# Kernel tuning notes

Hardware: AMD Instinct MI355X
Metric: run time of the kernel (lower is better)

## Reference

```python
import jax, jax.numpy as jnp
import numpy as np

D_MODEL = 2048
NUM_HEADS = 16
HEAD_DIM = D_MODEL // NUM_HEADS


def setup_inputs() -> dict:
    key = jax.random.key(0)
    ks = jax.random.split(key, 11)
    B, S = 2, 2048
    s = 1.0 / np.sqrt(D_MODEL)
    return {
        "query": jax.random.normal(ks[0], (B, S, D_MODEL), jnp.float32),
        "key_in": jax.random.normal(ks[1], (B, S, D_MODEL), jnp.float32),
        "value": jax.random.normal(ks[2], (B, S, D_MODEL), jnp.float32),
        "Wq": jax.random.normal(ks[3], (D_MODEL, D_MODEL), jnp.float32) * s,
        "bq": jnp.zeros((D_MODEL,), jnp.float32),
        "Wk": jax.random.normal(ks[4], (D_MODEL, D_MODEL), jnp.float32) * s,
        "bk": jnp.zeros((D_MODEL,), jnp.float32),
        "Wv": jax.random.normal(ks[5], (D_MODEL, D_MODEL), jnp.float32) * s,
        "bv": jnp.zeros((D_MODEL,), jnp.float32),
        "Wo": jax.random.normal(ks[6], (D_MODEL, D_MODEL), jnp.float32) * s,
        "bo": jnp.zeros((D_MODEL,), jnp.float32),
    }


def reference(query, key_in, value, Wq, bq, Wk, bk, Wv, bv, Wo, bo):
    B, S, _ = query.shape
    # projections (torch Linear: x @ W.T + b)
    q = query @ Wq.T + bq
    k = key_in @ Wk.T + bk
    v = value @ Wv.T + bv
    # [B, H, S, Dh]
    q = q.reshape(B, S, NUM_HEADS, HEAD_DIM).transpose(0, 2, 1, 3)
    k = k.reshape(B, -1, NUM_HEADS, HEAD_DIM).transpose(0, 2, 1, 3)
    v = v.reshape(B, -1, NUM_HEADS, HEAD_DIM).transpose(0, 2, 1, 3)
    scores = jnp.einsum("bhqd,bhkd->bhqk", q, k) / np.sqrt(HEAD_DIM).astype(np.float32)
    attn = jax.nn.softmax(scores, axis=-1)
    out = jnp.einsum("bhqk,bhkd->bhqd", attn, v)
    out = out.transpose(0, 2, 1, 3).reshape(B, S, D_MODEL)
    return out @ Wo.T + bo
```

## Files before the change

### kernel.cpp

```cpp
#include <hip/hip_runtime.h>
#include <hip/hip_bf16.h>
#include <stdint.h>

typedef __hip_bfloat16 bf16;
typedef __attribute__((ext_vector_type(8))) short bf16x8;
typedef __attribute__((ext_vector_type(4))) float f32x4;
typedef __attribute__((ext_vector_type(4))) short s16x4;

constexpr int D_MODEL   = 2048;
constexpr int NUM_HEADS = 16;
constexpr int HEAD_DIM  = 128;
constexpr int BATCH     = 2;
constexpr int SEQ       = 2048;

__device__ __forceinline__ void gload_lds16(const bf16* g, bf16* l) {
    __builtin_amdgcn_global_load_lds(
        (const __attribute__((address_space(1))) void*)g,
        (__attribute__((address_space(3))) void*)l, 16, 0, 0);
}

struct CvtArgs { const float* src[7]; bf16* dst[7]; int n8[7]; };

__global__ __launch_bounds__(256)
void cvt_multi(CvtArgs a)
{
    const int t = blockIdx.y;
    const float* __restrict__ s = a.src[t];
    bf16* __restrict__ d = a.dst[t];
    const int n8 = a.n8[t];
    for (int i = blockIdx.x * 256 + threadIdx.x; i < n8; i += gridDim.x * 256) {
        f32x4 x = *(const f32x4*)(s + (size_t)i * 8);
        f32x4 y = *(const f32x4*)(s + (size_t)i * 8 + 4);
        bf16 t8[8] = { __float2bfloat16(x[0]), __float2bfloat16(x[1]),
                       __float2bfloat16(x[2]), __float2bfloat16(x[3]),
                       __float2bfloat16(y[0]), __float2bfloat16(y[1]),
                       __float2bfloat16(y[2]), __float2bfloat16(y[3]) };
        *(bf16x8*)(d + (size_t)i * 8) = *(const bf16x8*)t8;
    }
}

template <typename TC, bool TRANS_PERM>
__device__ __forceinline__
void gemm_body(const bf16* __restrict__ A, const bf16* __restrict__ W,
               const float* __restrict__ bias, TC* __restrict__ C,
               int M, int N, int K)
{
    constexpr int BM = 128, BN = 128, BK = 32;
    __shared__ bf16 sA[BM][BK];
    __shared__ bf16 sB[BN][BK];

    const int tid  = threadIdx.x;
    const int wave = tid >> 6, lane = tid & 63;
    const int quad = lane >> 4, l16 = lane & 15;
    const int wr = wave >> 1, wc = wave & 1;
    const int m0 = blockIdx.y * BM, n0 = blockIdx.x * BN;
    bf16* sAf = &sA[0][0];
    bf16* sBf = &sB[0][0];

    f32x4 acc[4][4];
#pragma unroll
    for (int i = 0; i < 4; i++)
#pragma unroll
        for (int j = 0; j < 4; j++) acc[i][j] = (f32x4){0.f, 0.f, 0.f, 0.f};

    for (int k0 = 0; k0 < K; k0 += BK) {
        __syncthreads();
#pragma unroll
        for (int s = 0; s < 2; s++) {
            int c = s * 256 + wave * 64 + lane;
            int row = c >> 2, col = (c & 3) * 8;
            gload_lds16(&A[(size_t)(m0 + row) * K + k0 + col], sAf + (size_t)c * 8);
            gload_lds16(&W[(size_t)(n0 + row) * K + k0 + col], sBf + (size_t)c * 8);
        }
        __syncthreads();

        bf16x8 af[4], bfr[4];
#pragma unroll
        for (int i = 0; i < 4; i++) af[i]  = *(const bf16x8*)&sA[wr * 64 + i * 16 + l16][quad * 8];
#pragma unroll
        for (int j = 0; j < 4; j++) bfr[j] = *(const bf16x8*)&sB[wc * 64 + j * 16 + l16][quad * 8];
#pragma unroll
        for (int i = 0; i < 4; i++)
#pragma unroll
            for (int j = 0; j < 4; j++)
                acc[i][j] = __builtin_amdgcn_mfma_f32_16x16x32_bf16(af[i], bfr[j], acc[i][j], 0, 0, 0);
    }

#pragma unroll
    for (int j = 0; j < 4; j++) {
        int col = n0 + wc * 64 + j * 16 + l16;
        float bv = bias[col];
#pragma unroll
        for (int i = 0; i < 4; i++) {
            if constexpr (TRANS_PERM) {
                int row0 = m0 + wr * 64 + i * 16 + quad * 4;
                int g    = row0 & 63;
                int tau  = g >> 4, qh = (g >> 2) & 3;
                int pp   = (tau >> 1) * 32 + qh * 8 + (tau & 1) * 4;
                int sp   = ((row0 & 2047) & ~63) | pp;
                size_t idx = (size_t)(row0 >> 11) * ((size_t)D_MODEL * SEQ)
                           + (size_t)col * SEQ + sp;
                bf16 t4[4];
#pragma unroll
                for (int r = 0; r < 4; r++) t4[r] = __float2bfloat16(acc[i][j][r] + bv);
                *(s16x4*)&C[idx] = *(const s16x4*)t4;
            } else {
#pragma unroll
                for (int r = 0; r < 4; r++) {
                    int row = m0 + wr * 64 + i * 16 + quad * 4 + r;
                    if constexpr (sizeof(TC) == 2)
                        C[(size_t)row * N + col] = (TC)__float2bfloat16(acc[i][j][r] + bv);
                    else
                        C[(size_t)row * N + col] = (TC)(acc[i][j][r] + bv);
                }
            }
        }
    }
}

template <typename TC, bool TRANS_PERM>
__global__ __launch_bounds__(256, 2)
void gemm_bf16(const bf16* __restrict__ A, const bf16* __restrict__ W,
               const float* __restrict__ bias, TC* __restrict__ C,
               int M, int N, int K)
{
    gemm_body<TC, TRANS_PERM>(A, W, bias, C, M, N, K);
}

struct QkvArgs { const bf16* A[3]; const bf16* W[3]; const float* bias[3]; bf16* C[3]; };

__global__ __launch_bounds__(256, 2)
void gemm_qkv(QkvArgs ga, int M, int N, int K)
{
    const int z = blockIdx.z;
    if (z == 2) gemm_body<bf16, true >(ga.A[2], ga.W[2], ga.bias[2], ga.C[2], M, N, K);
    else        gemm_body<bf16, false>(ga.A[z], ga.W[z], ga.bias[z], ga.C[z], M, N, K);
}

struct QkArgs { const bf16* A[2]; const bf16* W[2]; const float* bias[2]; bf16* C[2]; };

__global__ __launch_bounds__(256, 2)
void gemm_qk(QkArgs ga, int M, int N, int K)
{
    const int z = blockIdx.z;
    gemm_body<bf16, false>(ga.A[z], ga.W[z], ga.bias[z], ga.C[z], M, N, K);
}

__global__ __launch_bounds__(256)
void flash_attn_kernel(const bf16* __restrict__ Qp, const bf16* __restrict__ Kp,
                       const bf16* __restrict__ Vt, bf16* __restrict__ Op)
{
    constexpr int BQ = 128, BKV = 64, DH = 128;
    __shared__ bf16 sK[2][BKV * DH];
    __shared__ bf16 sV[2][DH * BKV];

    const int tid  = threadIdx.x;
    const int wave = tid >> 6, lane = tid & 63;
    const int quad = lane >> 4, l16 = lane & 15;
    const int q0 = blockIdx.x * BQ;
    const int h  = blockIdx.y;
    const int b  = blockIdx.z;

    const size_t base  = (size_t)b * SEQ * D_MODEL + (size_t)h * HEAD_DIM;
    const size_t basev = ((size_t)b * NUM_HEADS + h) * (size_t)HEAD_DIM * SEQ;
    const bf16* Kb = Kp + base;
    const bf16* Vb = Vt + basev;

    auto stage = [&](int t, int bi) {
        const bf16* Kt = Kb + (size_t)t * BKV * D_MODEL;
        const bf16* Vtile = Vb + (size_t)t * BKV;
        bf16* sKb = sK[bi];
        bf16* sVb = sV[bi];
#pragma unroll
        for (int s = 0; s < 4; s++) {
            int c = s * 256 + wave * 64 + lane;
            int row = c >> 4, gs = c & 15;
            int g = gs ^ (row & 15);
            gload_lds16(Kt + (size_t)row * D_MODEL + g * 8, sKb + (size_t)c * 8);
        }
#pragma unroll
        for (int s = 0; s < 4; s++) {
            int c = s * 256 + wave * 64 + lane;
            int dh = c >> 3, gs = c & 7;
            int g = gs ^ (dh & 7);
            gload_lds16(Vtile + (size_t)dh * SEQ + g * 8, sVb + (size_t)c * 8);
        }
    };

    bf16x8 bq[2][4];
#pragma unroll
    for (int nt = 0; nt < 2; nt++)
#pragma unroll
        for (int kk = 0; kk < 4; kk++)
            bq[nt][kk] = *(const bf16x8*)&Qp[base +
                (size_t)(q0 + wave * 32 + nt * 16 + l16) * D_MODEL + kk * 32 + quad * 8];

    f32x4 oacc[2][8];
#pragma unroll
    for (int nt = 0; nt < 2; nt++)
#pragma unroll
        for (int mt = 0; mt < 8; mt++) oacc[nt][mt] = (f32x4){0.f, 0.f, 0.f, 0.f};

    float lsum[2] = {0.f, 0.f};

    const float SCL2E = 0.08838834764831845f * 1.4426950408889634f;
    constexpr int NT = SEQ / BKV;

    stage(0, 0);

    for (int t = 0; t < NT; ++t) {
        __syncthreads();
        if (t + 1 < NT) stage(t + 1, (t + 1) & 1);

        const bf16* sKc = sK[t & 1];
        const bf16* sVc = sV[t & 1];

        f32x4 sacc[2][4];
#pragma unroll
        for (int nt = 0; nt < 2; nt++)
#pragma unroll
            for (int kt = 0; kt < 4; kt++) sacc[nt][kt] = (f32x4){0.f, 0.f, 0.f, 0.f};
#pragma unroll
        for (int kk = 0; kk < 4; kk++) {
            bf16x8 ak[4];
#pragma unroll
            for (int kt = 0; kt < 4; kt++) {
                int row = kt * 16 + l16;
                int g   = (kk * 4 + quad) ^ l16;
                ak[kt] = *(const bf16x8*)&sKc[(size_t)row * DH + g * 8];
            }
#pragma unroll
            for (int nt = 0; nt < 2; nt++)
#pragma unroll
                for (int kt = 0; kt < 4; kt++)
                    sacc[nt][kt] = __builtin_amdgcn_mfma_f32_16x16x32_bf16(ak[kt], bq[nt][kk], sacc[nt][kt], 0, 0, 0);
        }

        bf16x8 pb[2][2];
#pragma unroll
        for (int nt = 0; nt < 2; nt++) {
            bf16 tmp[16];
#pragma unroll
            for (int kt = 0; kt < 4; kt++) {
#pragma unroll
                for (int r = 0; r < 4; r++) {
                    float p = exp2f(fminf(sacc[nt][kt][r] * SCL2E, 60.f));
                    lsum[nt] += p;
                    tmp[(kt >> 1) * 8 + (kt & 1) * 4 + r] = __float2bfloat16(p);
                }
            }
            pb[nt][0] = *(const bf16x8*)&tmp[0];
            pb[nt][1] = *(const bf16x8*)&tmp[8];
        }

#pragma unroll
        for (int c = 0; c < 2; c++) {
#pragma unroll
            for (int mt = 0; mt < 8; mt++) {
                int row = mt * 16 + l16;
                int g   = (c * 4 + quad) ^ (l16 & 7);
                bf16x8 av = *(const bf16x8*)&sVc[(size_t)row * BKV + g * 8];
#pragma unroll
                for (int nt = 0; nt < 2; nt++)
                    oacc[nt][mt] = __builtin_amdgcn_mfma_f32_16x16x32_bf16(av, pb[nt][c], oacc[nt][mt], 0, 0, 0);
            }
        }
    }

#pragma unroll
    for (int nt = 0; nt < 2; nt++) {
        float v = lsum[nt];
        v += __shfl_xor(v, 16);
        v += __shfl_xor(v, 32);
        lsum[nt] = v;
    }

#pragma unroll
    for (int nt = 0; nt < 2; nt++) {
        float inv = 1.f / lsum[nt];
        int row = q0 + wave * 32 + nt * 16 + l16;
#pragma unroll
        for (int mt = 0; mt < 8; mt++) {
            bf16 t4[4];
#pragma unroll
            for (int r = 0; r < 4; r++) t4[r] = __float2bfloat16(oacc[nt][mt][r] * inv);
            *(s16x4*)&Op[base + (size_t)row * D_MODEL + mt * 16 + quad * 4] = *(const s16x4*)t4;
        }
    }
}

extern "C" void kernel_launch(void* const* d_in, const int* in_sizes, int n_in,
                              void* d_out, int out_size, void* d_ws, size_t ws_size,
                              hipStream_t stream)
{
    const float* query  = (const float*)d_in[0];
    const float* key_in = (const float*)d_in[1];
    const float* value  = (const float*)d_in[2];
    const float* Wq = (const float*)d_in[3];
    const float* bq = (const float*)d_in[4];
    const float* Wk = (const float*)d_in[5];
    const float* bk = (const float*)d_in[6];
    const float* Wv = (const float*)d_in[7];
    const float* bv = (const float*)d_in[8];
    const float* Wo = (const float*)d_in[9];
    const float* bo = (const float*)d_in[10];
    float* out = (float*)d_out;

    const int tokens = BATCH * SEQ;
    const size_t nAct = (size_t)tokens * D_MODEL;
    const size_t nW   = (size_t)D_MODEL * D_MODEL;

    const bool fused_qkv = ws_size >= (6 * nAct + 4 * nW) * sizeof(bf16);

    bf16* p = (bf16*)d_ws;
    bf16* qb  = p; p += nAct;
    bf16* kb  = p; p += nAct;
    bf16* vb  = p; p += nAct;
    bf16* wqb = p; p += nW;
    bf16* wkb = p; p += nW;
    bf16* wvb = p; p += nW;
    bf16* wob = p; p += nW;
    bf16* qp  = p; p += nAct;
    bf16* kp  = p; p += nAct;
    bf16* vpT;
    if (fused_qkv) { vpT = p; p += nAct; }
    else           { vpT = qb; }
    bf16* ap = fused_qkv ? qb : kb;

    CvtArgs ca;
    ca.src[0] = query;  ca.dst[0] = qb;  ca.n8[0] = (int)(nAct / 8);
    ca.src[1] = key_in; ca.dst[1] = kb;  ca.n8[1] = (int)(nAct / 8);
    ca.src[2] = value;  ca.dst[2] = vb;  ca.n8[2] = (int)(nAct / 8);
    ca.src[3] = Wq;     ca.dst[3] = wqb; ca.n8[3] = (int)(nW / 8);
    ca.src[4] = Wk;     ca.dst[4] = wkb; ca.n8[4] = (int)(nW / 8);
    ca.src[5] = Wv;     ca.dst[5] = wvb; ca.n8[5] = (int)(nW / 8);
    ca.src[6] = Wo;     ca.dst[6] = wob; ca.n8[6] = (int)(nW / 8);
    cvt_multi<<<dim3(512, 7), 256, 0, stream>>>(ca);

    if (fused_qkv) {
        QkvArgs qa;
        qa.A[0] = qb; qa.W[0] = wqb; qa.bias[0] = bq; qa.C[0] = qp;
        qa.A[1] = kb; qa.W[1] = wkb; qa.bias[1] = bk; qa.C[1] = kp;
        qa.A[2] = vb; qa.W[2] = wvb; qa.bias[2] = bv; qa.C[2] = vpT;
        dim3 g3(D_MODEL / 128, tokens / 128, 3);
        gemm_qkv<<<g3, 256, 0, stream>>>(qa, tokens, D_MODEL, D_MODEL);
    } else {
        QkArgs qa;
        qa.A[0] = qb; qa.W[0] = wqb; qa.bias[0] = bq; qa.C[0] = qp;
        qa.A[1] = kb; qa.W[1] = wkb; qa.bias[1] = bk; qa.C[1] = kp;
        dim3 g2(D_MODEL / 128, tokens / 128, 2);
        gemm_qk<<<g2, 256, 0, stream>>>(qa, tokens, D_MODEL, D_MODEL);
        dim3 gg(D_MODEL / 128, tokens / 128);
        gemm_bf16<bf16, true><<<gg, 256, 0, stream>>>(vb, wvb, bv, vpT, tokens, D_MODEL, D_MODEL);
    }

    dim3 ga(SEQ / 128, NUM_HEADS, BATCH);
    flash_attn_kernel<<<ga, 256, 0, stream>>>(qp, kp, vpT, ap);

    dim3 gg(D_MODEL / 128, tokens / 128);
    gemm_bf16<float, false><<<gg, 256, 0, stream>>>(ap, wob, bo, out, tokens, D_MODEL, D_MODEL);
}
```

Before: 481.1 us.

## Rewrite projection GEMMs with 256x128 tiles, triple-buffered LDS and swizzled loads

Replaces the single-buffered 128x128x32 GEMM with a 512-thread 256x128x64 tile that triple-buffers A and B in LDS via direct global-to-LDS loads. Data for step t+2 is prefetched while four interleaved MFMA phases run, with XOR-swizzled LDS addressing to avoid bank conflicts and s_setprio around the MFMA bursts. The goal is to hide global load latency and cut the per-k-step barrier stalls of the old loop. In exchange each block uses much more LDS (about 144 KB) and registers, leaving one block per CU, and the grid has half as many blocks. Correctness rests on hand-placed vmcnt waits and barriers.

```diff
diff --git a/kernel.cpp b/kernel.cpp
--- a/kernel.cpp
+++ b/kernel.cpp
@@ -12,6 +12,12 @@
 constexpr int HEAD_DIM  = 128;
 constexpr int BATCH     = 2;
 constexpr int SEQ       = 2048;
+
+constexpr int GBM = 256, GBN = 128, GBK = 64;
+constexpr int G_ABUF = GBM * GBK;
+constexpr int G_BBUF = GBN * GBK;
+constexpr int G_BUF  = G_ABUF + G_BBUF;
+constexpr int G_LDS  = 3 * G_BUF;
 
 __device__ __forceinline__ void gload_lds16(const bf16* g, bf16* l) {
     __builtin_amdgcn_global_load_lds(
@@ -39,23 +45,52 @@
     }
 }
 
+template <int P>
+__device__ __forceinline__
+void phase_mfma(f32x4 (&acc)[4][4], bf16x8 (&a)[4][2], bf16x8 (&b)[4][2])
+{
+#pragma unroll
+    for (int kk = 0; kk < 2; kk++) {
+#pragma unroll
+        for (int j = 0; j <= P; j++)
+            acc[P][j] = __builtin_amdgcn_mfma_f32_16x16x32_bf16(a[P][kk], b[j][kk], acc[P][j], 0, 0, 0);
+#pragma unroll
+        for (int i = 0; i < P; i++)
+            acc[i][P] = __builtin_amdgcn_mfma_f32_16x16x32_bf16(a[i][kk], b[P][kk], acc[i][P], 0, 0, 0);
+    }
+}
+
 template <typename TC, bool TRANS_PERM>
 __device__ __forceinline__
 void gemm_body(const bf16* __restrict__ A, const bf16* __restrict__ W,
                const float* __restrict__ bias, TC* __restrict__ C,
-               int M, int N, int K)
-{
-    constexpr int BM = 128, BN = 128, BK = 32;
-    __shared__ bf16 sA[BM][BK];
-    __shared__ bf16 sB[BN][BK];
-
+               int M, int N, int K, bf16* smem)
+{
     const int tid  = threadIdx.x;
-    const int wave = tid >> 6, lane = tid & 63;
+    const int lane = tid & 63;
+    const int wave = tid >> 6;
     const int quad = lane >> 4, l16 = lane & 15;
-    const int wr = wave >> 1, wc = wave & 1;
-    const int m0 = blockIdx.y * BM, n0 = blockIdx.x * BN;
-    bf16* sAf = &sA[0][0];
-    bf16* sBf = &sB[0][0];
+    const int sw   = l16 & 7;
+    const int wr   = wave >> 1;
+    const int wc   = wave & 1;
+    const int m0   = blockIdx.y * GBM, n0 = blockIdx.x * GBN;
+
+    const int rloc = tid >> 3;
+    const int gsw  = (tid & 7) ^ (rloc & 7);
+    const int NT   = K / GBK;
+
+    const bf16* Abase = A + (size_t)(m0 + rloc) * K + gsw * 8;
+    const bf16* Bbase = W + (size_t)(n0 + rloc) * K + gsw * 8;
+    const size_t rstep = (size_t)64 * K;
+
+    auto stageA = [&](int t, int bi, int u) {
+        gload_lds16(Abase + u * rstep + (size_t)t * GBK,
+                    smem + bi * G_BUF + (u * 512 + tid) * 8);
+    };
+    auto stageB = [&](int t, int bi, int u) {
+        gload_lds16(Bbase + u * rstep + (size_t)t * GBK,
+                    smem + bi * G_BUF + G_ABUF + (u * 512 + tid) * 8);
+    };
 
     f32x4 acc[4][4];
 #pragma unroll
@@ -63,41 +98,71 @@
 #pragma unroll
         for (int j = 0; j < 4; j++) acc[i][j] = (f32x4){0.f, 0.f, 0.f, 0.f};
 
-    for (int k0 = 0; k0 < K; k0 += BK) {
-        __syncthreads();
-#pragma unroll
-        for (int s = 0; s < 2; s++) {
-            int c = s * 256 + wave * 64 + lane;
-            int row = c >> 2, col = (c & 3) * 8;
-            gload_lds16(&A[(size_t)(m0 + row) * K + k0 + col], sAf + (size_t)c * 8);
-            gload_lds16(&W[(size_t)(n0 + row) * K + k0 + col], sBf + (size_t)c * 8);
-        }
-        __syncthreads();
-
-        bf16x8 af[4], bfr[4];
-#pragma unroll
-        for (int i = 0; i < 4; i++) af[i]  = *(const bf16x8*)&sA[wr * 64 + i * 16 + l16][quad * 8];
-#pragma unroll
-        for (int j = 0; j < 4; j++) bfr[j] = *(const bf16x8*)&sB[wc * 64 + j * 16 + l16][quad * 8];
-#pragma unroll
-        for (int i = 0; i < 4; i++)
-#pragma unroll
-            for (int j = 0; j < 4; j++)
-                acc[i][j] = __builtin_amdgcn_mfma_f32_16x16x32_bf16(af[i], bfr[j], acc[i][j], 0, 0, 0);
-    }
+    bf16x8 a[4][2], b[4][2];
+
+#pragma unroll
+    for (int u = 0; u < 4; u++) stageA(0, 0, u);
+#pragma unroll
+    for (int u = 0; u < 2; u++) stageB(0, 0, u);
+    if (NT > 1) {
+#pragma unroll
+        for (int u = 0; u < 4; u++) stageA(1, 1, u);
+#pragma unroll
+        for (int u = 0; u < 2; u++) stageB(1, 1, u);
+        asm volatile("s_waitcnt vmcnt(6)" ::: "memory");
+    } else {
+        asm volatile("s_waitcnt vmcnt(0)" ::: "memory");
+    }
+    asm volatile("s_barrier" ::: "memory");
+
+#define GEMM_PHASE(p, STAGE_STMT)                                              \
+    {                                                                          \
+        STAGE_STMT;                                                            \
+        const int rA = wr * 64 + (p) * 16 + l16;                               \
+        const int rB = wc * 64 + (p) * 16 + l16;                               \
+        a[p][0] = *(const bf16x8*)&sAc[rA * 64 + (quad ^ sw) * 8];             \
+        a[p][1] = *(const bf16x8*)&sAc[rA * 64 + (((4 + quad) ^ sw)) * 8];     \
+        b[p][0] = *(const bf16x8*)&sBc[rB * 64 + (quad ^ sw) * 8];             \
+        b[p][1] = *(const bf16x8*)&sBc[rB * 64 + (((4 + quad) ^ sw)) * 8];     \
+        __builtin_amdgcn_s_barrier();                                          \
+        __builtin_amdgcn_s_setprio(1);                                         \
+        phase_mfma<p>(acc, a, b);                                              \
+        __builtin_amdgcn_s_setprio(0);                                         \
+    }
+
+    int bc = 0;
+    for (int t = 0; t < NT; ++t) {
+        const bf16* sAc = smem + bc * G_BUF;
+        const bf16* sBc = sAc + G_ABUF;
+        const int bs = (bc + 2 >= 3) ? bc - 1 : bc + 2;
+        const bool pf = (t + 2 < NT);
+
+        GEMM_PHASE(0, if (pf) { stageA(t + 2, bs, 0); stageA(t + 2, bs, 1); })
+        __builtin_amdgcn_s_barrier();
+        GEMM_PHASE(1, if (pf) { stageA(t + 2, bs, 2); stageA(t + 2, bs, 3); })
+        __builtin_amdgcn_s_barrier();
+        GEMM_PHASE(2, if (pf) { stageB(t + 2, bs, 0); })
+        __builtin_amdgcn_s_barrier();
+        GEMM_PHASE(3, if (pf) { stageB(t + 2, bs, 1); })
+        if (pf)                asm volatile("s_waitcnt vmcnt(6)" ::: "memory");
+        else if (t + 1 < NT)   asm volatile("s_waitcnt vmcnt(0)" ::: "memory");
+        asm volatile("s_barrier" ::: "memory");
+        bc = (bc + 1 == 3) ? 0 : bc + 1;
+    }
+#undef GEMM_PHASE
 
 #pragma unroll
     for (int j = 0; j < 4; j++) {
-        int col = n0 + wc * 64 + j * 16 + l16;
-        float bv = bias[col];
+        const int col = n0 + wc * 64 + j * 16 + l16;
+        const float bv = bias[col];
 #pragma unroll
         for (int i = 0; i < 4; i++) {
+            const int row0 = m0 + wr * 64 + i * 16 + quad * 4;
             if constexpr (TRANS_PERM) {
-                int row0 = m0 + wr * 64 + i * 16 + quad * 4;
-                int g    = row0 & 63;
-                int tau  = g >> 4, qh = (g >> 2) & 3;
-                int pp   = (tau >> 1) * 32 + qh * 8 + (tau & 1) * 4;
-                int sp   = ((row0 & 2047) & ~63) | pp;
+                int g   = row0 & 63;
+                int tau = g >> 4, qh = (g >> 2) & 3;
+                int pp  = (tau >> 1) * 32 + qh * 8 + (tau & 1) * 4;
+                int sp  = ((row0 & 2047) & ~63) | pp;
                 size_t idx = (size_t)(row0 >> 11) * ((size_t)D_MODEL * SEQ)
                            + (size_t)col * SEQ + sp;
                 bf16 t4[4];
@@ -107,7 +172,7 @@
             } else {
 #pragma unroll
                 for (int r = 0; r < 4; r++) {
-                    int row = m0 + wr * 64 + i * 16 + quad * 4 + r;
+                    int row = row0 + r;
                     if constexpr (sizeof(TC) == 2)
                         C[(size_t)row * N + col] = (TC)__float2bfloat16(acc[i][j][r] + bv);
                     else
@@ -119,31 +184,34 @@
 }
 
 template <typename TC, bool TRANS_PERM>
-__global__ __launch_bounds__(256, 2)
+__global__ __launch_bounds__(512, 1)
 void gemm_bf16(const bf16* __restrict__ A, const bf16* __restrict__ W,
                const float* __restrict__ bias, TC* __restrict__ C,
                int M, int N, int K)
 {
-    gemm_body<TC, TRANS_PERM>(A, W, bias, C, M, N, K);
+    __shared__ bf16 smem[G_LDS];
+    gemm_body<TC, TRANS_PERM>(A, W, bias, C, M, N, K, smem);
 }
 
 struct QkvArgs { const bf16* A[3]; const bf16* W[3]; const float* bias[3]; bf16* C[3]; };
 
-__global__ __launch_bounds__(256, 2)
+__global__ __launch_bounds__(512, 1)
 void gemm_qkv(QkvArgs ga, int M, int N, int K)
 {
+    __shared__ bf16 smem[G_LDS];
     const int z = blockIdx.z;
-    if (z == 2) gemm_body<bf16, true >(ga.A[2], ga.W[2], ga.bias[2], ga.C[2], M, N, K);
-    else        gemm_body<bf16, false>(ga.A[z], ga.W[z], ga.bias[z], ga.C[z], M, N, K);
+    if (z == 2) gemm_body<bf16, true >(ga.A[2], ga.W[2], ga.bias[2], ga.C[2], M, N, K, smem);
+    else        gemm_body<bf16, false>(ga.A[z], ga.W[z], ga.bias[z], ga.C[z], M, N, K, smem);
 }
 
 struct QkArgs { const bf16* A[2]; const bf16* W[2]; const float* bias[2]; bf16* C[2]; };
 
-__global__ __launch_bounds__(256, 2)
+__global__ __launch_bounds__(512, 1)
 void gemm_qk(QkArgs ga, int M, int N, int K)
 {
+    __shared__ bf16 smem[G_LDS];
     const int z = blockIdx.z;
-    gemm_body<bf16, false>(ga.A[z], ga.W[z], ga.bias[z], ga.C[z], M, N, K);
+    gemm_body<bf16, false>(ga.A[z], ga.W[z], ga.bias[z], ga.C[z], M, N, K, smem);
 }
 
 __global__ __launch_bounds__(256)
@@ -342,21 +410,21 @@
         qa.A[0] = qb; qa.W[0] = wqb; qa.bias[0] = bq; qa.C[0] = qp;
         qa.A[1] = kb; qa.W[1] = wkb; qa.bias[1] = bk; qa.C[1] = kp;
         qa.A[2] = vb; qa.W[2] = wvb; qa.bias[2] = bv; qa.C[2] = vpT;
-        dim3 g3(D_MODEL / 128, tokens / 128, 3);
-        gemm_qkv<<<g3, 256, 0, stream>>>(qa, tokens, D_MODEL, D_MODEL);
+        dim3 g3(D_MODEL / 128, tokens / 256, 3);
+        gemm_qkv<<<g3, 512, 0, stream>>>(qa, tokens, D_MODEL, D_MODEL);
     } else {
         QkArgs qa;
         qa.A[0] = qb; qa.W[0] = wqb; qa.bias[0] = bq; qa.C[0] = qp;
         qa.A[1] = kb; qa.W[1] = wkb; qa.bias[1] = bk; qa.C[1] = kp;
-        dim3 g2(D_MODEL / 128, tokens / 128, 2);
-        gemm_qk<<<g2, 256, 0, stream>>>(qa, tokens, D_MODEL, D_MODEL);
-        dim3 gg(D_MODEL / 128, tokens / 128);
-        gemm_bf16<bf16, true><<<gg, 256, 0, stream>>>(vb, wvb, bv, vpT, tokens, D_MODEL, D_MODEL);
+        dim3 g2(D_MODEL / 128, tokens / 256, 2);
+        gemm_qk<<<g2, 512, 0, stream>>>(qa, tokens, D_MODEL, D_MODEL);
+        dim3 gg(D_MODEL / 128, tokens / 256);
+        gemm_bf16<bf16, true><<<gg, 512, 0, stream>>>(vb, wvb, bv, vpT, tokens, D_MODEL, D_MODEL);
     }
 
     dim3 ga(SEQ / 128, NUM_HEADS, BATCH);
     flash_attn_kernel<<<ga, 256, 0, stream>>>(qp, kp, vpT, ap);
 
-    dim3 gg(D_MODEL / 128, tokens / 128);
-    gemm_bf16<float, false><<<gg, 256, 0, stream>>>(ap, wob, bo, out, tokens, D_MODEL, D_MODEL);
-}
+    dim3 gg(D_MODEL / 128, tokens / 256);
+    gemm_bf16<float, false><<<gg, 512, 0, stream>>>(ap, wob, bo, out, tokens, D_MODEL, D_MODEL);
+}
```

After: 488.6 us. About the same (+1.6%).
